# Kernel optimization log

Hardware: AMD Instinct MI355X
Metric: run time of the kernel (lower is better)

## Reference

```python
import jax, jax.numpy as jnp
import numpy as np

B, M, N, C, H = 2, 2048, 2048, 1024, 16
HD = C // H  # head dim = 64


def setup_inputs() -> dict:
    key = jax.random.key(0)
    ks = jax.random.split(key, 8)
    std = 0.25
    return {
        "x": jax.random.normal(ks[0], (B, M, C), dtype=jnp.float32),
        "data": jax.random.normal(ks[1], (B, N, C), dtype=jnp.float32),
        # weights stored [in, out] (transpose of torch Linear weight)
        "W_attn": jax.random.normal(ks[2], (C, 3 * C), dtype=jnp.float32) * std,
        "b_attn": jnp.zeros((3 * C,), dtype=jnp.float32),
        "W_data": jax.random.normal(ks[3], (C, 2 * C), dtype=jnp.float32) * std,
        "b_data": jnp.zeros((2 * C,), dtype=jnp.float32),
        "W_proj": jax.random.normal(ks[4], (C, C), dtype=jnp.float32) * std,
        "b_proj": jnp.zeros((C,), dtype=jnp.float32),
    }


def reference(x, data, W_attn, b_attn, W_data, b_data, W_proj, b_proj):
    # QKV from queries x: [B, M, 3, C] -> q, k, v each [B, M, C]
    qkv = (x @ W_attn + b_attn).reshape(B, M, 3, C)
    q, k, v = qkv[:, :, 0], qkv[:, :, 1], qkv[:, :, 2]
    # KV from data: [B, N, 2, C]
    kv = (data @ W_data + b_data).reshape(B, N, 2, C)
    k_data, v_data = kv[:, :, 0], kv[:, :, 1]
    # concat self KV with data KV along sequence -> length T = M + N
    k = jnp.concatenate([k, k_data], axis=1)
    v = jnp.concatenate([v, v_data], axis=1)
    T = M + N
    # split heads
    qh = q.reshape(B, M, H, HD).transpose(0, 2, 1, 3)  # [B,H,M,HD]
    kh = k.reshape(B, T, H, HD).transpose(0, 2, 1, 3)  # [B,H,T,HD]
    vh = v.reshape(B, T, H, HD).transpose(0, 2, 1, 3)  # [B,H,T,HD]
    scale = 1.0 / np.sqrt(HD).astype(np.float32)
    attn = jax.nn.softmax(jnp.einsum("bhmd,bhtd->bhmt", qh, kh) * scale, axis=-1)
    out = jnp.einsum("bhmt,bhtd->bhmd", attn, vh)  # [B,H,M,HD]
    out = out.transpose(0, 2, 1, 3).reshape(B, M, C)
    return out @ W_proj + b_proj
```

## Files before the change

kernel.cpp:

```cpp
#include <hip/hip_runtime.h>

typedef __bf16 bf16x8 __attribute__((ext_vector_type(8)));
typedef __bf16 bf16x4 __attribute__((ext_vector_type(4)));
typedef _Float16 f16x8 __attribute__((ext_vector_type(8)));
typedef float f32x4 __attribute__((ext_vector_type(4)));
typedef float f32x16 __attribute__((ext_vector_type(16)));
typedef unsigned short u16x8 __attribute__((ext_vector_type(8)));
typedef unsigned short u16x4 __attribute__((ext_vector_type(4)));
typedef unsigned int u32x4 __attribute__((ext_vector_type(4)));
typedef unsigned short us;

#define MM 2048
#define TT 4096

__device__ __forceinline__ us f2bf(float f){
  unsigned int u = __builtin_bit_cast(unsigned int, f);
  u = (u + 0x7fffu + ((u >> 16) & 1u)) >> 16;
  return (us)u;
}
__device__ __forceinline__ float bf2f(us u){
  unsigned int x = ((unsigned int)u) << 16;
  return __builtin_bit_cast(float, x);
}
__device__ __forceinline__ us f2h(float f){
  _Float16 h = (_Float16)f;
  return __builtin_bit_cast(us, h);
}
__device__ __forceinline__ unsigned int cvt_pk_bf16(float lo, float hi){
  unsigned int r;
  asm("v_cvt_pk_bf16_f32 %0, %1, %2" : "=v"(r) : "v"(lo), "v"(hi));
  return r;
}
__device__ __forceinline__ void plane_swap(unsigned int &x, unsigned int &y){
  asm("v_permlane32_swap_b32 %0, %1" : "+v"(x), "+v"(y));
}
__device__ __forceinline__ float fast_exp2(float s, float A23, float B23){
  float t = __builtin_fmaf(s, A23, B23);
  t = fmaxf(t, 0.f);
  return __builtin_bit_cast(float, (int)t);
}

#define GLDS(gp, lp) __builtin_amdgcn_global_load_lds( \
    (const __attribute__((address_space(1))) unsigned int*)(gp), \
    (__attribute__((address_space(3))) unsigned int*)(lp), 16, 0, 0)

__global__ __launch_bounds__(256) void cast_f16_all(const float* __restrict__ x,
                                                    const float* __restrict__ data,
                                                    us* __restrict__ xf, us* __restrict__ df){
  int bid = blockIdx.x;
  const float* in; us* o;
  if (bid < 2048){ in = x; o = xf; }
  else           { in = data; o = df; bid -= 2048; }
  size_t i = ((size_t)bid * 256 + threadIdx.x) * 8;
  float4 a = *(const float4*)(in + i);
  float4 b = *(const float4*)(in + i + 4);
  float v[8] = {a.x,a.y,a.z,a.w,b.x,b.y,b.z,b.w};
  u16x8 r;
  for (int j = 0; j < 8; j++) r[j] = f2h(v[j]);
  *(u16x8*)(o + i) = r;
}

__global__ __launch_bounds__(256) void transpose_all(const float* __restrict__ W_attn,
                                                     const float* __restrict__ W_data,
                                                     const float* __restrict__ W_proj,
                                                     us* __restrict__ Af, us* __restrict__ Df,
                                                     us* __restrict__ Pb){
  __shared__ float tile[32][33];
  int bx = blockIdx.x;
  const float* W; us* o; int N; bool tobf;
  if (bx < 96){ W = W_attn; o = Af; N = 3072; tobf = false; }
  else if (bx < 160){ W = W_data; o = Df; N = 2048; bx -= 96; tobf = false; }
  else { W = W_proj; o = Pb; N = 1024; bx -= 160; tobf = true; }
  int tx = threadIdx.x & 31, ty = threadIdx.x >> 5;
  int n0 = bx * 32, k0 = blockIdx.y * 32;
  for (int r = 0; r < 32; r += 8)
    tile[ty + r][tx] = W[(size_t)(k0 + ty + r) * N + n0 + tx];
  __syncthreads();
  for (int r = 0; r < 32; r += 8){
    float v = tile[tx][ty + r];
    size_t idx = (size_t)(n0 + ty + r) * 1024 + k0 + tx;
    o[idx] = tobf ? f2bf(v) : f2h(v);
  }
}

__global__ __launch_bounds__(256) void gemm_all(const us* __restrict__ xf, const us* __restrict__ df,
                                                const us* __restrict__ Watf, const us* __restrict__ Wdtf,
                                                const float* __restrict__ b_attn, const float* __restrict__ b_data,
                                                us* __restrict__ Qf, us* __restrict__ Kf,
                                                us* __restrict__ VT){
  __shared__ us sm[8192];
  const int bx = blockIdx.x;
  const us *Ah, *Bth; const float* bias; int region, kroff, col0;
  if (bx < 24){
    Ah = xf; Bth = Watf; bias = b_attn;
    region = bx >> 3; kroff = 0; col0 = bx * 128;
  } else {
    int b2 = bx - 24;
    Ah = df; Bth = Wdtf; bias = b_data;
    region = 1 + (b2 >> 3); kroff = 2048; col0 = b2 * 128;
  }
  const int tid = threadIdx.x, wid = tid >> 6, lane = tid & 63;
  const int l15 = lane & 15, l16 = lane >> 4;
  const int row0 = blockIdx.y * 128;
  const int wr = (wid >> 1) * 64, wc = (wid & 1) * 64;
  f32x4 acc[4][4] = {};

  for (int k0 = 0; k0 < 1024; k0 += 32){
    for (int c = 0; c < 2; ++c){
      int i = c * 256 + tid;
      size_t aoff = (size_t)(row0 + (i >> 2)) * 1024 + k0 + (i & 3) * 8;
      size_t boff = (size_t)(col0 + (i >> 2)) * 1024 + k0 + (i & 3) * 8;
      GLDS(Ah + aoff, &sm[c * 2048 + wid * 512]);
      GLDS(Bth + boff, &sm[4096 + c * 2048 + wid * 512]);
    }
    __syncthreads();
    f16x8 af[4], bf[4];
    for (int m = 0; m < 4; m++) af[m] = *(const f16x8*)&sm[(wr + m * 16 + l15) * 32 + l16 * 8];
    for (int n = 0; n < 4; n++) bf[n] = *(const f16x8*)&sm[4096 + (wc + n * 16 + l15) * 32 + l16 * 8];
    for (int m = 0; m < 4; m++)
      for (int n = 0; n < 4; n++)
        acc[m][n] = __builtin_amdgcn_mfma_f32_16x16x32_f16(af[m], bf[n], acc[m][n], 0, 0, 0);
    __syncthreads();
  }

  for (int m = 0; m < 4; m++)
    for (int n = 0; n < 4; n++){
      int gcol = col0 + wc + n * 16 + l15;
      int ocol = gcol & 1023;
      float bv = bias[gcol];
      if (region == 2){
        int r = row0 + wr + m * 16 + l16 * 4;
        u16x4 o;
        for (int j = 0; j < 4; j++) o[j] = f2bf(acc[m][n][j] + bv);
        *(u16x4*)&VT[((size_t)((r >> 11) * 1024 + ocol)) * 4096 + kroff + (r & 2047)] = o;
      } else {
        us* P = (region == 0) ? Qf : Kf;
        for (int j = 0; j < 4; j++){
          int r = row0 + wr + m * 16 + l16 * 4 + j;
          size_t orow = (region == 0) ? (size_t)r
                                      : (size_t)((r >> 11) * 4096 + kroff + (r & 2047));
          P[orow * 1024 + ocol] = f2h(acc[m][n][j] + bv);
        }
      }
    }
}

__global__ __launch_bounds__(256) void gemm_proj(const us* __restrict__ Ah,
                                                 const us* __restrict__ Bth,
                                                 const float* __restrict__ bias,
                                                 float* __restrict__ Co){
  __shared__ us sm[8192];
  const int tid = threadIdx.x, wid = tid >> 6, lane = tid & 63;
  const int l15 = lane & 15, l16 = lane >> 4;
  const int row0 = blockIdx.y * 128, col0 = blockIdx.x * 128;
  const int wr = (wid >> 1) * 64, wc = (wid & 1) * 64;
  f32x4 acc[4][4] = {};

  for (int k0 = 0; k0 < 1024; k0 += 32){
    for (int c = 0; c < 2; ++c){
      int i = c * 256 + tid;
      size_t aoff = (size_t)(row0 + (i >> 2)) * 1024 + k0 + (i & 3) * 8;
      size_t boff = (size_t)(col0 + (i >> 2)) * 1024 + k0 + (i & 3) * 8;
      GLDS(Ah + aoff, &sm[c * 2048 + wid * 512]);
      GLDS(Bth + boff, &sm[4096 + c * 2048 + wid * 512]);
    }
    __syncthreads();
    bf16x8 afh[4], bfh[4];
    for (int m = 0; m < 4; m++) afh[m] = *(const bf16x8*)&sm[(wr + m * 16 + l15) * 32 + l16 * 8];
    for (int n = 0; n < 4; n++) bfh[n] = *(const bf16x8*)&sm[4096 + (wc + n * 16 + l15) * 32 + l16 * 8];
    for (int m = 0; m < 4; m++)
      for (int n = 0; n < 4; n++)
        acc[m][n] = __builtin_amdgcn_mfma_f32_16x16x32_bf16(afh[m], bfh[n], acc[m][n], 0, 0, 0);
    __syncthreads();
  }

  for (int m = 0; m < 4; m++)
    for (int n = 0; n < 4; n++){
      int col = col0 + wc + n * 16 + l15;
      float bv = bias[col];
      for (int j = 0; j < 4; j++){
        int r = row0 + wr + m * 16 + l16 * 4 + j;
        Co[(size_t)r * 1024 + col] = acc[m][n][j] + bv;
      }
    }
}

__global__ __launch_bounds__(256) void attn_kernel(const us* __restrict__ Qf,
                                                   const us* __restrict__ Kf,
                                                   const us* __restrict__ VT,
                                                   us* __restrict__ attno){
  __shared__ us Kb[2][64 * 72];
  __shared__ us Vb[2][64 * 72];
  const int tid = threadIdx.x, wid = tid >> 6, lane = tid & 63;
  const int l31 = lane & 31, hb = lane >> 5, h8 = hb * 8;
  const int qt = blockIdx.x & 15;
  const int bh = blockIdx.x >> 4;
  const int hd = (bh & 15) * 64, b = bh >> 4;
  const int qrow = qt * 128 + wid * 32 + l31;

  f16x8 qf[4];
  {
    const us* qp = Qf + (size_t)(b * MM + qrow) * 1024 + hd;
#pragma unroll
    for (int kk = 0; kk < 4; kk++)
      qf[kk] = *(const f16x8*)(qp + kk * 16 + h8);
  }

  u16x8 ones_u;
#pragma unroll
  for (int j = 0; j < 8; j++) ones_u[j] = 0x3F80;
  const bf16x8 ones8 = __builtin_bit_cast(bf16x8, ones_u);

  const int i0 = tid, i1 = 256 + tid;
  const int kt0 = i0 >> 3, kd0 = (i0 & 7) * 8;
  const int kt1 = i1 >> 3, kd1 = (i1 & 7) * 8;

#define GK(t0_, t_, d_) (((size_t)(b * TT + (t0_) + (t_))) * 1024 + hd + (d_))
#define GV(t0_, d_, t_) (((size_t)b * 1024 + hd + (d_)) * 4096 + (t0_) + (t_))

  uint4 rK0 = *(const uint4*)(Kf + GK(0, kt0, kd0));
  uint4 rK1 = *(const uint4*)(Kf + GK(0, kt1, kd1));
  uint4 rV0 = *(const uint4*)(VT + GV(0, kt0, kd0));
  uint4 rV1 = *(const uint4*)(VT + GV(0, kt1, kd1));
  *(uint4*)&Kb[0][kt0 * 72 + kd0] = rK0;
  *(uint4*)&Kb[0][kt1 * 72 + kd1] = rK1;
  *(uint4*)&Vb[0][kt0 * 72 + kd0] = rV0;
  *(uint4*)&Vb[0][kt1 * 72 + kd1] = rV1;
  __syncthreads();

  f32x16 acc0 = {}, acc1 = {}, accS = {};
  float mrow = -1e30f;
  const float cs  = 0.125f * 1.44269504088896f;
  const float A23 = cs * 8388608.0f;
  float B23 = 0.f;

  for (int t0 = 0; t0 < TT; t0 += 64){
    const int cur = (t0 >> 6) & 1;
    const bool pre = (t0 + 64 < TT);
    if (pre){
      rK0 = *(const uint4*)(Kf + GK(t0 + 64, kt0, kd0));
      rK1 = *(const uint4*)(Kf + GK(t0 + 64, kt1, kd1));
      rV0 = *(const uint4*)(VT + GV(t0 + 64, kt0, kd0));
      rV1 = *(const uint4*)(VT + GV(t0 + 64, kt1, kd1));
    }

    const us* KbC = &Kb[cur][0];
    f32x16 sfr0 = {}, sfr1 = {};
    __builtin_amdgcn_s_setprio(1);
#pragma unroll
    for (int kk = 0; kk < 4; kk++){
      f16x8 a0 = *(const f16x8*)&KbC[l31 * 72 + kk * 16 + h8];
      f16x8 a1 = *(const f16x8*)&KbC[(32 + l31) * 72 + kk * 16 + h8];
      sfr0 = __builtin_amdgcn_mfma_f32_32x32x16_f16(a0, qf[kk], sfr0, 0, 0, 0);
      sfr1 = __builtin_amdgcn_mfma_f32_32x32x16_f16(a1, qf[kk], sfr1, 0, 0, 0);
    }
    __builtin_amdgcn_s_setprio(0);

    float va = -1e30f, vb2 = -1e30f;
#pragma unroll
    for (int r = 0; r < 16; r += 2){
      va  = fmaxf(fmaxf(sfr0[r],     sfr1[r]),     va);
      vb2 = fmaxf(fmaxf(sfr0[r + 1], sfr1[r + 1]), vb2);
    }
    float v = fmaxf(va, vb2);
    float vs = v * cs;
    vs = fmaxf(vs, __shfl_xor(vs, 32, 64));
    if (!__all(vs <= mrow + 8.f)){
      float mn = fmaxf(mrow, vs);
      float rs = __builtin_amdgcn_exp2f(mrow - mn);
      mrow = mn;
#pragma unroll
      for (int r = 0; r < 16; r++){ acc0[r] *= rs; acc1[r] *= rs; accS[r] *= rs; }
    }
    B23 = __builtin_fmaf(mrow, -8388608.0f, 1065103216.0f);
    unsigned int A0[4][2], A1[4][2];
#pragma unroll
    for (int g = 0; g < 4; g++){
      float e00 = fast_exp2(sfr0[4*g+0], A23, B23);
      float e01 = fast_exp2(sfr0[4*g+1], A23, B23);
      float e02 = fast_exp2(sfr0[4*g+2], A23, B23);
      float e03 = fast_exp2(sfr0[4*g+3], A23, B23);
      float e10 = fast_exp2(sfr1[4*g+0], A23, B23);
      float e11 = fast_exp2(sfr1[4*g+1], A23, B23);
      float e12 = fast_exp2(sfr1[4*g+2], A23, B23);
      float e13 = fast_exp2(sfr1[4*g+3], A23, B23);
      A0[g][0] = cvt_pk_bf16(e00, e01);
      A0[g][1] = cvt_pk_bf16(e02, e03);
      A1[g][0] = cvt_pk_bf16(e10, e11);
      A1[g][1] = cvt_pk_bf16(e12, e13);
    }

    bf16x8 pf[4];
#pragma unroll
    for (int kkl = 0; kkl < 2; kkl++){
      unsigned int x0 = A0[2*kkl][0], y0 = A0[2*kkl+1][0];
      unsigned int x1 = A0[2*kkl][1], y1 = A0[2*kkl+1][1];
      plane_swap(x0, y0);
      plane_swap(x1, y1);
      u32x4 w = {x0, x1, y0, y1};
      pf[kkl] = __builtin_bit_cast(bf16x8, w);
      unsigned int z0 = A1[2*kkl][0], t0w = A1[2*kkl+1][0];
      unsigned int z1 = A1[2*kkl][1], t1w = A1[2*kkl+1][1];
      plane_swap(z0, t0w);
      plane_swap(z1, t1w);
      u32x4 w2 = {z0, z1, t0w, t1w};
      pf[2 + kkl] = __builtin_bit_cast(bf16x8, w2);
    }

    const us* VbC = &Vb[cur][0];
    __builtin_amdgcn_s_setprio(1);
#pragma unroll
    for (int kk = 0; kk < 4; kk++){
      bf16x8 av0 = *(const bf16x8*)&VbC[l31 * 72 + kk * 16 + h8];
      bf16x8 av1 = *(const bf16x8*)&VbC[(32 + l31) * 72 + kk * 16 + h8];
      acc0 = __builtin_amdgcn_mfma_f32_32x32x16_bf16(av0, pf[kk], acc0, 0, 0, 0);
      acc1 = __builtin_amdgcn_mfma_f32_32x32x16_bf16(av1, pf[kk], acc1, 0, 0, 0);
      accS = __builtin_amdgcn_mfma_f32_32x32x16_bf16(ones8, pf[kk], accS, 0, 0, 0);
    }
    __builtin_amdgcn_s_setprio(0);

    if (pre){
      const int nxt = cur ^ 1;
      *(uint4*)&Kb[nxt][kt0 * 72 + kd0] = rK0;
      *(uint4*)&Kb[nxt][kt1 * 72 + kd1] = rK1;
      *(uint4*)&Vb[nxt][kt0 * 72 + kd0] = rV0;
      *(uint4*)&Vb[nxt][kt1 * 72 + kd1] = rV1;
    }
    __syncthreads();
  }
#undef GK
#undef GV

  float inv = 1.f / accS[0];
  us* op = attno + (size_t)(b * MM + qrow) * 1024 + hd;
#pragma unroll
  for (int g = 0; g < 4; g++){
    bf16x4 w0, w1;
#pragma unroll
    for (int j = 0; j < 4; j++){
      w0[j] = (__bf16)(acc0[4 * g + j] * inv);
      w1[j] = (__bf16)(acc1[4 * g + j] * inv);
    }
    *(u16x4*)&op[8 * g + 4 * hb]      = __builtin_bit_cast(u16x4, w0);
    *(u16x4*)&op[32 + 8 * g + 4 * hb] = __builtin_bit_cast(u16x4, w1);
  }
}

extern "C" void kernel_launch(void* const* d_in, const int* in_sizes, int n_in,
                              void* d_out, int out_size, void* d_ws, size_t ws_size,
                              hipStream_t stream){
  const float* x      = (const float*)d_in[0];
  const float* data   = (const float*)d_in[1];
  const float* W_attn = (const float*)d_in[2];
  const float* b_attn = (const float*)d_in[3];
  const float* W_data = (const float*)d_in[4];
  const float* b_data = (const float*)d_in[5];
  const float* W_proj = (const float*)d_in[6];
  const float* b_proj = (const float*)d_in[7];
  float* out = (float*)d_out;

  char* ws = (char*)d_ws;
  us* xf    = (us*)(ws + 0);
  us* df    = (us*)(ws + 8388608);
  us* Watf  = (us*)(ws + 16777216);
  us* Wdtf  = (us*)(ws + 23068672);
  us* Wptb  = (us*)(ws + 27262976);
  us* Qf    = (us*)(ws + 29360128);
  us* Kf    = (us*)(ws + 37748736);
  us* VT    = (us*)(ws + 54525952);
  us* attno = (us*)(ws + 0);

  cast_f16_all<<<4096, 256, 0, stream>>>(x, data, xf, df);
  transpose_all<<<dim3(192, 32), 256, 0, stream>>>(W_attn, W_data, W_proj, Watf, Wdtf, Wptb);

  gemm_all<<<dim3(40, 32), 256, 0, stream>>>(xf, df, Watf, Wdtf,
                                             b_attn, b_data, Qf, Kf, VT);

  attn_kernel<<<512, 256, 0, stream>>>(Qf, Kf, VT, attno);

  gemm_proj<<<dim3(8, 32), 256, 0, stream>>>(attno, Wptb, b_proj, out);
}
```

Measured before the change: 237.3 us.

## Split attention over two key-sequence chunks with a separate combine kernel

Each attention block now handles half of the key/value sequence (split-K flash-decoding style). The grid doubles from 512 to 1024 blocks to fill the MI355X compute units better. Unnormalized partial outputs, row maxima and row sums go to workspace, and a new combine kernel rescales and merges the two halves. This adds a kernel launch, extra global memory traffic for the partials, and bf16 rounding of the unnormalized accumulators.

```diff
diff --git a/kernel.cpp b/kernel.cpp
--- a/kernel.cpp
+++ b/kernel.cpp
@@ -185,18 +185,21 @@
     }
 }
 
-__global__ __launch_bounds__(256) void attn_kernel(const us* __restrict__ Qf,
-                                                   const us* __restrict__ Kf,
-                                                   const us* __restrict__ VT,
-                                                   us* __restrict__ attno){
+__global__ __launch_bounds__(256, 4) void attn_kernel(const us* __restrict__ Qf,
+                                                      const us* __restrict__ Kf,
+                                                      const us* __restrict__ VT,
+                                                      us* __restrict__ accP,
+                                                      float* __restrict__ Mv, float* __restrict__ Lv){
   __shared__ us Kb[2][64 * 72];
   __shared__ us Vb[2][64 * 72];
   const int tid = threadIdx.x, wid = tid >> 6, lane = tid & 63;
   const int l31 = lane & 31, hb = lane >> 5, h8 = hb * 8;
   const int qt = blockIdx.x & 15;
-  const int bh = blockIdx.x >> 4;
+  const int bh = (blockIdx.x >> 4) & 31;
+  const int tch = blockIdx.x >> 9;
   const int hd = (bh & 15) * 64, b = bh >> 4;
   const int qrow = qt * 128 + wid * 32 + l31;
+  const int tbase = tch * 2048, tend = tbase + 2048;
 
   f16x8 qf[4];
   {
@@ -218,10 +221,10 @@
 #define GK(t0_, t_, d_) (((size_t)(b * TT + (t0_) + (t_))) * 1024 + hd + (d_))
 #define GV(t0_, d_, t_) (((size_t)b * 1024 + hd + (d_)) * 4096 + (t0_) + (t_))
 
-  uint4 rK0 = *(const uint4*)(Kf + GK(0, kt0, kd0));
-  uint4 rK1 = *(const uint4*)(Kf + GK(0, kt1, kd1));
-  uint4 rV0 = *(const uint4*)(VT + GV(0, kt0, kd0));
-  uint4 rV1 = *(const uint4*)(VT + GV(0, kt1, kd1));
+  uint4 rK0 = *(const uint4*)(Kf + GK(tbase, kt0, kd0));
+  uint4 rK1 = *(const uint4*)(Kf + GK(tbase, kt1, kd1));
+  uint4 rV0 = *(const uint4*)(VT + GV(tbase, kt0, kd0));
+  uint4 rV1 = *(const uint4*)(VT + GV(tbase, kt1, kd1));
   *(uint4*)&Kb[0][kt0 * 72 + kd0] = rK0;
   *(uint4*)&Kb[0][kt1 * 72 + kd1] = rK1;
   *(uint4*)&Vb[0][kt0 * 72 + kd0] = rV0;
@@ -234,9 +237,9 @@
   const float A23 = cs * 8388608.0f;
   float B23 = 0.f;
 
-  for (int t0 = 0; t0 < TT; t0 += 64){
+  for (int t0 = tbase; t0 < tend; t0 += 64){
     const int cur = (t0 >> 6) & 1;
-    const bool pre = (t0 + 64 < TT);
+    const bool pre = (t0 + 64 < tend);
     if (pre){
       rK0 = *(const uint4*)(Kf + GK(t0 + 64, kt0, kd0));
       rK1 = *(const uint4*)(Kf + GK(t0 + 64, kt1, kd1));
@@ -331,19 +334,47 @@
 #undef GK
 #undef GV
 
-  float inv = 1.f / accS[0];
-  us* op = attno + (size_t)(b * MM + qrow) * 1024 + hd;
+  us* ap = accP + (size_t)tch * 4194304 + (size_t)(b * MM + qrow) * 1024 + hd;
 #pragma unroll
   for (int g = 0; g < 4; g++){
     bf16x4 w0, w1;
 #pragma unroll
     for (int j = 0; j < 4; j++){
-      w0[j] = (__bf16)(acc0[4 * g + j] * inv);
-      w1[j] = (__bf16)(acc1[4 * g + j] * inv);
-    }
-    *(u16x4*)&op[8 * g + 4 * hb]      = __builtin_bit_cast(u16x4, w0);
-    *(u16x4*)&op[32 + 8 * g + 4 * hb] = __builtin_bit_cast(u16x4, w1);
-  }
+      w0[j] = (__bf16)acc0[4 * g + j];
+      w1[j] = (__bf16)acc1[4 * g + j];
+    }
+    *(u16x4*)&ap[8 * g + 4 * hb]      = __builtin_bit_cast(u16x4, w0);
+    *(u16x4*)&ap[32 + 8 * g + 4 * hb] = __builtin_bit_cast(u16x4, w1);
+  }
+  if (hb == 0){
+    int idx = tch * 65536 + (b * MM + qrow) * 16 + (hd >> 6);
+    Mv[idx] = mrow;
+    Lv[idx] = accS[0];
+  }
+}
+
+__global__ __launch_bounds__(256) void combine_kernel(const us* __restrict__ accP,
+                                                      const float* __restrict__ Mv,
+                                                      const float* __restrict__ Lv,
+                                                      us* __restrict__ attno){
+  size_t i = ((size_t)blockIdx.x * 256 + threadIdx.x) * 8;
+  size_t qg = i >> 10;
+  int h = (int)((i & 1023) >> 6);
+  size_t mi = qg * 16 + h;
+  float m1 = Mv[mi], m2 = Mv[65536 + mi];
+  float l1 = Lv[mi], l2 = Lv[65536 + mi];
+  float m = fmaxf(m1, m2);
+  float w1 = __builtin_amdgcn_exp2f(m1 - m);
+  float w2 = __builtin_amdgcn_exp2f(m2 - m);
+  float inv = 1.f / (w1 * l1 + w2 * l2);
+  float s1 = w1 * inv, s2 = w2 * inv;
+  u16x8 a1 = *(const u16x8*)(accP + i);
+  u16x8 a2 = *(const u16x8*)(accP + 4194304 + i);
+  u16x8 o;
+#pragma unroll
+  for (int j = 0; j < 8; j++)
+    o[j] = f2bf(s1 * bf2f(a1[j]) + s2 * bf2f(a2[j]));
+  *(u16x8*)(attno + i) = o;
 }
 
 extern "C" void kernel_launch(void* const* d_in, const int* in_sizes, int n_in,
@@ -368,6 +399,9 @@
   us* Qf    = (us*)(ws + 29360128);
   us* Kf    = (us*)(ws + 37748736);
   us* VT    = (us*)(ws + 54525952);
+  us* accP  = (us*)(ws + 71303168);
+  float* Mv = (float*)(ws + 88080384);
+  float* Lv = (float*)(ws + 88604672);
   us* attno = (us*)(ws + 0);
 
   cast_f16_all<<<4096, 256, 0, stream>>>(x, data, xf, df);
@@ -376,7 +410,8 @@
   gemm_all<<<dim3(40, 32), 256, 0, stream>>>(xf, df, Watf, Wdtf,
                                              b_attn, b_data, Qf, Kf, VT);
 
-  attn_kernel<<<512, 256, 0, stream>>>(Qf, Kf, VT, attno);
+  attn_kernel<<<1024, 256, 0, stream>>>(Qf, Kf, VT, accP, Mv, Lv);
+  combine_kernel<<<2048, 256, 0, stream>>>(accP, Mv, Lv, attno);
 
   gemm_proj<<<dim3(8, 32), 256, 0, stream>>>(attno, Wptb, b_proj, out);
 }
```

Result: faster. 228.7 us (-3.6%).
